# Kernel tuning notes

Hardware: AMD Instinct MI355X
Metric: run time of the kernel (lower is better)

The kernel has to match this reference:

```python
import jax, jax.numpy as jnp
import numpy as np

N, E, H, NH, RBF_K = 512, 4096, 128, 8, 64
CUTOFF = 10.0
HH = H * NH  # 1024


def setup_inputs() -> dict:
    key = jax.random.key(0)
    ks = jax.random.split(key, 30)
    def lin_w(k, fan_in, fan_out):
        return jax.random.normal(k, (fan_in, fan_out), jnp.float32) * (fan_in ** -0.5)
    inp = {
        'atom_embs': jax.random.normal(ks[0], (N, H), jnp.float32),
        'pos': jax.random.normal(ks[1], (N, 3), jnp.float32),
        'edge_weight': jax.random.normal(ks[2], (E,), jnp.float32),
        'edge_indices': jax.random.randint(ks[3], (2, E), 0, N, jnp.int64),
        'Wq': lin_w(ks[4], H, HH),
        'Wk': lin_w(ks[5], H, HH),
        'Wv': lin_w(ks[6], H, HH),
        'li_w': lin_w(ks[7], H, H), 'li_b': jnp.zeros((H,), jnp.float32),
        'lj_w': lin_w(ks[8], H, H), 'lj_b': jnp.zeros((H,), jnp.float32),
        'el_w': lin_w(ks[9], 3 * H, HH), 'el_b': jnp.zeros((HH,), jnp.float32),
        'rl_w': lin_w(ks[10], RBF_K, HH), 'rl_b': jnp.zeros((HH,), jnp.float32),
        'ol_w': lin_w(ks[11], HH, H), 'ol_b': jnp.zeros((H,), jnp.float32),
        'ln_g': jnp.ones((H,), jnp.float32), 'ln_b': jnp.zeros((H,), jnp.float32),
        'f1_w': lin_w(ks[12], H, H), 'f1_b': jnp.zeros((H,), jnp.float32),
        'f2_w': lin_w(ks[13], H, H), 'f2_b': jnp.zeros((H,), jnp.float32),
        'f3_w': lin_w(ks[14], H, H), 'f3_b': jnp.zeros((H,), jnp.float32),
    }
    return inp


def _scatter_softmax_cols(logits, seg, num_segments):
    # softmax over columns of `logits` grouped by seg (column -> source node)
    lt = logits.T                                   # [E_cols, E_rows]
    m = jax.ops.segment_max(lt, seg, num_segments=num_segments)
    e = jnp.exp(lt - m[seg])
    s = jax.ops.segment_sum(e, seg, num_segments=num_segments)
    return (e / s[seg]).T


def _rbf(d):
    # d: [E, 1]. ExponentialRBF with softplus(softplus_inverse(x)) == x identities
    centers = jnp.linspace(1.0, np.exp(-CUTOFF).astype(np.float32), RBF_K)
    widths = np.float32((0.5 / ((1.0 - np.exp(-CUTOFF)) / RBF_K)) ** 2)
    x = d / CUTOFF
    x3 = x ** 3; x4 = x3 * x; x5 = x4 * x
    cut = jnp.where(x < 1, 1 - 6 * x5 + 15 * x4 - 10 * x3, jnp.zeros_like(x))
    return cut * jnp.exp(-widths * (jnp.exp(-d) - centers) ** 2)   # [E, K]


def reference(atom_embs, pos, edge_weight, edge_indices, Wq, Wk, Wv,
              li_w, li_b, lj_w, lj_b, el_w, el_b, rl_w, rl_b, ol_w, ol_b,
              ln_g, ln_b, f1_w, f1_b, f2_w, f2_b, f3_w, f3_b):
    src, tgt = edge_indices[0], edge_indices[1]
    ew = edge_weight[:, None]
    ai = atom_embs[tgt] + ew                      # atom_embs_i (+= edge_weight)
    aj = atom_embs[src] + ew                      # atom_embs_j (+= edge_weight)
    Q = ai @ Wq
    K = ai @ Wk
    V = ai @ Wv                                   # [E, HH]
    logits = (Q @ K.T) * (H ** -0.5)              # [E, E]
    prod = _scatter_softmax_cols(logits, src, N)  # scatter_softmax over edge_indices[0]
    hi = ai @ li_w + li_b
    hj = aj @ lj_w + lj_b
    edge_ij = jnp.concatenate([hi + hj, hi - hj, hi * hj], axis=-1)  # [E, 3H]
    d = jnp.linalg.norm(pos[tgt] - pos[src], axis=-1)[:, None]       # [E, 1]
    feats = edge_ij @ el_w + el_b + _rbf(d) @ rl_w + rl_b + V        # [E, HH]
    msg = (prod @ feats) @ ol_w + ol_b            # [E, H]
    agg = jax.ops.segment_sum(msg, tgt, num_segments=N)              # [N, H]

    def ln(x):
        mu = jnp.mean(x, -1, keepdims=True)
        var = jnp.var(x, -1, keepdims=True)
        return (x - mu) / jnp.sqrt(var + 1e-5) * ln_g + ln_b

    h = ln(agg)
    sp = jax.nn.softplus
    h = sp(sp(sp(h @ f1_w + f1_b) @ f2_w + f2_b) @ f3_w + f3_b)
    return ln(h)
```

## Files before the change

kernel.cpp:

```cpp
#include <hip/hip_runtime.h>
#include <math.h>

#define N_NODES 512
#define NE      4096
#define H       128
#define HH      1024
#define RBFK    64
#define KCAT    576
#define ALPHA   0.08838834764831845f

typedef __attribute__((ext_vector_type(8))) short bf16x8;
typedef __attribute__((ext_vector_type(4))) float f32x4;
typedef __attribute__((ext_vector_type(4))) short short4v;

__device__ __forceinline__ short f2bf(float x) {
    unsigned u = __builtin_bit_cast(unsigned, x);
    unsigned r = u + 0x7FFFu + ((u >> 16) & 1u);
    return (short)(r >> 16);
}
__device__ __forceinline__ float bf2f(short s) {
    return __builtin_bit_cast(float, ((unsigned)(unsigned short)s) << 16);
}

__device__ __forceinline__ void gload16(const short* g, short* l) {
    __builtin_amdgcn_global_load_lds(
        (const __attribute__((address_space(1))) void*)g,
        (__attribute__((address_space(3))) void*)l, 16, 0, 0);
}

#define RA 524288
#define RB 589824
#define RBZ 65536
#define RW 262144
#define RCW 2048
#define RD 131072
#define RE 32768
#define RG 65536
#define RF 512
#define RTOT (RA+RB+RBZ+RW+RCW+RD+RE+RG+RF)
#define PREP_BLOCKS (RTOT / 512 + 1)

__global__ __launch_bounds__(512) void k_prep(
    const int* __restrict__ ei, const float* __restrict__ ew,
    const float* __restrict__ atom_embs, const float* __restrict__ pos,
    const float* __restrict__ Wq, const float* __restrict__ Wk, const float* __restrict__ Wv,
    const float* __restrict__ li_w, const float* __restrict__ lj_w,
    const float* __restrict__ el_w, const float* __restrict__ rl_w,
    const float* __restrict__ ol_w, const float* __restrict__ el_b, const float* __restrict__ rl_b,
    int* __restrict__ srcO, int* __restrict__ tgtO, int* __restrict__ rankS,
    int* __restrict__ idxT, int* __restrict__ segStart, int* __restrict__ segStartT,
    int* __restrict__ nsegp,
    short* __restrict__ Acat, short* __restrict__ ajB, short* __restrict__ BcatT,
    short* __restrict__ WqkT, float* __restrict__ cwq, float* __restrict__ cwk,
    short* __restrict__ olT, short* __restrict__ liT, short* __restrict__ ljT,
    short* __restrict__ embB, float* __restrict__ cvec4)
{
    __shared__ int sh[4 * N_NODES];
    __shared__ int flag;
    const int t = threadIdx.x;
    if (t < 64) {
        int vv = ei[2 * t + 1];
        unsigned long long m = __ballot(vv != 0);
        if (t == 0) flag = (m == 0ULL);
    }
    __syncthreads();
    const int is64 = flag;

    if (blockIdx.x == 0) {
        int* hS = sh;
        int* hT = sh + N_NODES;
        int* sS = sh + 2 * N_NODES;
        int* sT = sh + 3 * N_NODES;
        hS[t] = 0; hT[t] = 0;
        __syncthreads();
        for (int e = t; e < NE; e += 512) {
            int s = is64 ? ei[2 * e]          : ei[e];
            int g = is64 ? ei[2 * NE + 2 * e] : ei[NE + e];
            srcO[e] = s; tgtO[e] = g;
            atomicAdd(&hS[s], 1);
            atomicAdd(&hT[g], 1);
        }
        __syncthreads();
        int cs = hS[t], ct = hT[t];
        sS[t] = cs; sT[t] = ct;
        __syncthreads();
        for (int off = 1; off < N_NODES; off <<= 1) {
            int a = (t >= off) ? sS[t - off] : 0;
            int b = (t >= off) ? sT[t - off] : 0;
            __syncthreads();
            sS[t] += a; sT[t] += b;
            __syncthreads();
        }
        segStart[t + 1]  = sS[t];
        segStartT[t + 1] = sT[t];
        if (t == 0) { segStart[0] = 0; segStartT[0] = 0; }
        hS[t] = sS[t] - cs;
        hT[t] = sT[t] - ct;
        sS[t] = (cs > 0) ? 1 : 0;
        __syncthreads();
        for (int off = 256; off > 0; off >>= 1) {
            if (t < off) sS[t] += sS[t + off];
            __syncthreads();
        }
        if (t == 0) nsegp[0] = sS[0];
        for (int e = t; e < NE; e += 512) {
            int s = is64 ? ei[2 * e]          : ei[e];
            int g = is64 ? ei[2 * NE + 2 * e] : ei[NE + e];
            int p = atomicAdd(&hS[s], 1);
            rankS[e] = p;
            int q = atomicAdd(&hT[g], 1);
            idxT[q] = e;
        }
        return;
    }

    int idx = (blockIdx.x - 1) * 512 + t;
    if (idx < RA) {
        int p = idx >> 7, h = idx & 127;
        int s  = is64 ? ei[2 * p]          : ei[p];
        int tg = is64 ? ei[2 * NE + 2 * p] : ei[NE + p];
        float w = ew[p];
        Acat[(size_t)p * KCAT + h] = f2bf(atom_embs[tg * H + h] + w);
        ajB[idx] = f2bf(atom_embs[s * H + h] + w);
        if (h < RBFK) {
            float dx = pos[tg * 3 + 0] - pos[s * 3 + 0];
            float dy = pos[tg * 3 + 1] - pos[s * 3 + 1];
            float dz = pos[tg * 3 + 2] - pos[s * 3 + 2];
            float d = sqrtf(dx * dx + dy * dy + dz * dz);
            float x = d * 0.1f;
            float cut = 0.0f;
            if (x < 1.0f) {
                float x3 = x * x * x, x4 = x3 * x, x5 = x4 * x;
                cut = 1.0f - 6.0f * x5 + 15.0f * x4 - 10.0f * x3;
            }
            float ck = 1.0f + (float)h * (-0.015872295239210119f);
            float tt = expf(-d) - ck;
            Acat[(size_t)p * KCAT + 512 + h] = f2bf(cut * expf(-1024.0929857f * tt * tt));
        }
        return;
    }
    idx -= RA;
    if (idx < RB) {
        int k = idx >> 10, n = idx & 1023;
        float v = (k < 128) ? Wv[k * HH + n]
                : (k < 512) ? el_w[(k - 128) * HH + n]
                            : rl_w[(k - 512) * HH + n];
        BcatT[idx] = f2bf(v);
        return;
    }
    idx -= RB;
    if (idx < RBZ) { BcatT[RB + idx] = 0; return; }
    idx -= RBZ;
    if (idx < RW) {
        int n = idx >> 7, k = idx & 127;
        float v = (n < 1024) ? Wq[k * HH + n] : Wk[k * HH + (n - 1024)];
        WqkT[idx] = f2bf(v);
        return;
    }
    idx -= RW;
    if (idx < RCW) {
        int which = idx >> 10, j = idx & 1023;
        const float* W = which ? Wk : Wq;
        float s = 0.0f;
        for (int k = 0; k < H; k++) s += W[k * HH + j];
        (which ? cwk : cwq)[j] = s;
        return;
    }
    idx -= RCW;
    if (idx < RD) {
        int h = idx >> 10, n = idx & 1023;
        olT[idx] = f2bf(ol_w[n * H + h]);
        return;
    }
    idx -= RD;
    if (idx < RE) {
        int which = idx >> 14, r = idx & 16383;
        int n = r >> 7, k = r & 127;
        (which ? ljT : liT)[r] = f2bf((which ? lj_w : li_w)[k * H + n]);
        return;
    }
    idx -= RE;
    if (idx < RG) { embB[idx] = f2bf(atom_embs[idx]); return; }
    idx -= RG;
    {
        int h = idx & 127, chunk = idx >> 7;
        float acc = 0.0f;
        int n0 = chunk * 256;
        for (int n = n0; n < n0 + 256; n++)
            acc += (el_b[n] + rl_b[n]) * ol_w[n * H + h];
        cvec4[idx] = acc;
    }
}

__device__ __forceinline__ void gemm_body(
    short* As, short* Bs,
    const short* __restrict__ A, int lda,
    const short* __restrict__ B, int ldb,
    void* __restrict__ Cp, int ldc,
    int kbeg, int kend, float alpha, const float* __restrict__ bias,
    long zoff_pitch, int out_mode, int row0, int col0)
{
    const int tid = threadIdx.x;
    const int wave = tid >> 6, lane = tid & 63;

    f32x4 acc[4][4];
#pragma unroll
    for (int i = 0; i < 4; i++)
#pragma unroll
        for (int j = 0; j < 4; j++) acc[i][j] = (f32x4){0.f, 0.f, 0.f, 0.f};

    const int m0 = (wave >> 1) * 64, n0 = (wave & 1) * 64;
    const int lr = lane >> 3;
    const int lc = (lane & 7) * 8;
    const int cl = lane & 15, quad = lane >> 4;

    for (int k0 = kbeg; k0 < kend; k0 += 64) {
#pragma unroll
        for (int i = 0; i < 4; i++) {
            int r = wave * 32 + i * 8;
            gload16(A + (size_t)(row0 + r + lr) * lda + k0 + lc, As + r * 64);
            gload16(B + (size_t)(col0 + r + lr) * ldb + k0 + lc, Bs + r * 64);
        }
        __syncthreads();
#pragma unroll
        for (int kk = 0; kk < 64; kk += 32) {
            bf16x8 af[4], bf[4];
            int ko = kk + quad * 8;
#pragma unroll
            for (int i = 0; i < 4; i++)
                af[i] = *(const bf16x8*)(As + (m0 + i * 16 + cl) * 64 + ko);
#pragma unroll
            for (int j = 0; j < 4; j++)
                bf[j] = *(const bf16x8*)(Bs + (n0 + j * 16 + cl) * 64 + ko);
#pragma unroll
            for (int i = 0; i < 4; i++)
#pragma unroll
                for (int j = 0; j < 4; j++)
                    acc[i][j] = __builtin_amdgcn_mfma_f32_16x16x32_bf16(af[i], bf[j], acc[i][j], 0, 0, 0);
        }
        __syncthreads();
    }

    if (out_mode == 1) {
        short* C = (short*)Cp;
#pragma unroll
        for (int i = 0; i < 4; i++)
#pragma unroll
            for (int j = 0; j < 4; j++) {
                int cc = col0 + n0 + j * 16 + cl;
                float bv = bias ? bias[cc] : 0.0f;
#pragma unroll
                for (int reg = 0; reg < 4; reg++) {
                    int rr = row0 + m0 + i * 16 + quad * 4 + reg;
                    C[(size_t)rr * ldc + cc] = f2bf(acc[i][j][reg] * alpha + bv);
                }
            }
    } else if (out_mode == 3) {
        short* C = (short*)Cp;
#pragma unroll
        for (int i = 0; i < 4; i++)
#pragma unroll
            for (int j = 0; j < 4; j++) {
                int cc = col0 + n0 + j * 16 + cl;
                int rr = row0 + m0 + i * 16 + quad * 4;
                short4v pack;
#pragma unroll
                for (int reg = 0; reg < 4; reg++) pack[reg] = f2bf(acc[i][j][reg] * alpha);
                *(short4v*)(C + (size_t)cc * ldc + rr) = pack;
            }
    } else {
        float* C = (float*)Cp + zoff_pitch;
#pragma unroll
        for (int i = 0; i < 4; i++)
#pragma unroll
            for (int j = 0; j < 4; j++) {
                int cc = col0 + n0 + j * 16 + cl;
#pragma unroll
                for (int reg = 0; reg < 4; reg++) {
                    int rr = row0 + m0 + i * 16 + quad * 4 + reg;
                    C[(size_t)rr * ldc + cc] = acc[i][j][reg] * alpha;
                }
            }
    }
}

__global__ __launch_bounds__(256) void k_gemm(
    const short* __restrict__ A, int lda,
    const short* __restrict__ B, int ldb,
    void* __restrict__ Cp, int ldc,
    int K, float alpha, const float* __restrict__ bias,
    long split_pitch, int out_mode)
{
    __shared__ __align__(16) short As[128 * 64];
    __shared__ __align__(16) short Bs[128 * 64];
    int kchunk = K / gridDim.z;
    gemm_body(As, Bs, A, lda, B, ldb, Cp, ldc,
              kchunk * blockIdx.z, kchunk * (blockIdx.z + 1), alpha, bias,
              (long)blockIdx.z * split_pitch, out_mode,
              blockIdx.y * 128, blockIdx.x * 128);
}

__device__ __forceinline__ void edgefeat_body(
    short* As, short* Bs, int row0,
    const short* __restrict__ Acat_in, const short* __restrict__ ajB,
    const short* __restrict__ liT, const short* __restrict__ ljT,
    const float* __restrict__ li_b, const float* __restrict__ lj_b,
    short* __restrict__ Acat)
{
    const int tid = threadIdx.x;
    const int wave = tid >> 6, lane = tid & 63;
    const int cl = lane & 15, quad = lane >> 4;
    const int m0 = (wave >> 1) * 64, n0 = (wave & 1) * 64;
    const int sr = lane >> 4, sc = (lane & 15) * 8;

    f32x4 ai_acc[4][4], aj_acc[4][4];
#pragma unroll
    for (int i = 0; i < 4; i++)
#pragma unroll
        for (int j = 0; j < 4; j++) {
            ai_acc[i][j] = (f32x4){0.f, 0.f, 0.f, 0.f};
            aj_acc[i][j] = (f32x4){0.f, 0.f, 0.f, 0.f};
        }

#pragma unroll
    for (int i = 0; i < 8; i++) {
        int r = wave * 32 + i * 4;
        gload16(Acat_in + (size_t)(row0 + r + sr) * KCAT + sc, As + r * 128);
        gload16(liT + (r + sr) * 128 + sc, Bs + r * 128);
    }
    __syncthreads();
#pragma unroll
    for (int kk = 0; kk < 128; kk += 32) {
        bf16x8 af[4], bf[4];
        int ko = kk + quad * 8;
#pragma unroll
        for (int i = 0; i < 4; i++) af[i] = *(const bf16x8*)(As + (m0 + i * 16 + cl) * 128 + ko);
#pragma unroll
        for (int j = 0; j < 4; j++) bf[j] = *(const bf16x8*)(Bs + (n0 + j * 16 + cl) * 128 + ko);
#pragma unroll
        for (int i = 0; i < 4; i++)
#pragma unroll
            for (int j = 0; j < 4; j++)
                ai_acc[i][j] = __builtin_amdgcn_mfma_f32_16x16x32_bf16(af[i], bf[j], ai_acc[i][j], 0, 0, 0);
    }
    __syncthreads();
#pragma unroll
    for (int i = 0; i < 8; i++) {
        int r = wave * 32 + i * 4;
        gload16(ajB + (size_t)(row0 + r + sr) * 128 + sc, As + r * 128);
        gload16(ljT + (r + sr) * 128 + sc, Bs + r * 128);
    }
    __syncthreads();
#pragma unroll
    for (int kk = 0; kk < 128; kk += 32) {
        bf16x8 af[4], bf[4];
        int ko = kk + quad * 8;
#pragma unroll
        for (int i = 0; i < 4; i++) af[i] = *(const bf16x8*)(As + (m0 + i * 16 + cl) * 128 + ko);
#pragma unroll
        for (int j = 0; j < 4; j++) bf[j] = *(const bf16x8*)(Bs + (n0 + j * 16 + cl) * 128 + ko);
#pragma unroll
        for (int i = 0; i < 4; i++)
#pragma unroll
            for (int j = 0; j < 4; j++)
                aj_acc[i][j] = __builtin_amdgcn_mfma_f32_16x16x32_bf16(af[i], bf[j], aj_acc[i][j], 0, 0, 0);
    }
#pragma unroll
    for (int i = 0; i < 4; i++)
#pragma unroll
        for (int j = 0; j < 4; j++) {
            int cc = n0 + j * 16 + cl;
            float bi = li_b[cc], bj = lj_b[cc];
#pragma unroll
            for (int reg = 0; reg < 4; reg++) {
                int rr = row0 + m0 + i * 16 + quad * 4 + reg;
                float hv = ai_acc[i][j][reg] + bi;
                float gv = aj_acc[i][j][reg] + bj;
                short* rowp = Acat + (size_t)rr * KCAT;
                rowp[128 + cc] = f2bf(hv + gv);
                rowp[256 + cc] = f2bf(hv - gv);
                rowp[384 + cc] = f2bf(hv * gv);
            }
        }
}

__global__ __launch_bounds__(256) void k_big(
    const short* __restrict__ Acat_in, const short* __restrict__ ajB,
    const short* __restrict__ liT, const short* __restrict__ ljT,
    const float* __restrict__ li_b, const float* __restrict__ lj_b,
    short* __restrict__ Acat,
    const short* __restrict__ embB, const short* __restrict__ WqkT,
    short* __restrict__ QKB,
    const short* __restrict__ olT, const short* __restrict__ BcatT,
    short* __restrict__ W2T)
{
    __shared__ __align__(16) char smem[65536];
    if (blockIdx.x < 32) {
        edgefeat_body((short*)smem, (short*)(smem + 32768), blockIdx.x * 128,
                      Acat_in, ajB, liT, ljT, li_b, lj_b, Acat);
    } else if (blockIdx.x < 96) {
        int id = blockIdx.x - 32;
        gemm_body((short*)smem, (short*)(smem + 16384),
                  embB, H, WqkT, H, QKB, 2048, 0, H, 1.0f, nullptr, 0, 1,
                  (id >> 4) * 128, (id & 15) * 128);
    } else {
        int id = blockIdx.x - 96;
        gemm_body((short*)smem, (short*)(smem + 16384),
                  olT, HH, BcatT, HH, W2T, 640, 0, HH, 1.0f, nullptr, 0, 1,
                  0, id * 128);
    }
}

__global__ __launch_bounds__(256) void k_zr(
    const short* __restrict__ QKB,
    const float* __restrict__ cwq, const float* __restrict__ cwk,
    const short* __restrict__ Acat, const short* __restrict__ W2T,
    short* __restrict__ GT,
    float* __restrict__ Z, float* __restrict__ pv, float* __restrict__ qv,
    float* __restrict__ sv)
{
    __shared__ __align__(16) char smem[32768];
    if (blockIdx.x < 32) {
        int zs = blockIdx.x >> 4;
        int tile = blockIdx.x & 15;
        gemm_body((short*)smem, (short*)(smem + 16384),
                  QKB, 2048, QKB + 1024, 2048, Z, N_NODES,
                  zs * 512, zs * 512 + 512, ALPHA, nullptr,
                  (long)zs * ((long)N_NODES * N_NODES), 0,
                  (tile >> 2) * 128, (tile & 3) * 128);
    } else if (blockIdx.x < 64) {
        int id = blockIdx.x - 32;
        gemm_body((short*)smem, (short*)(smem + 16384),
                  Acat, KCAT, W2T, 640, GT, NE, 0, KCAT, 1.0f, nullptr, 0, 3,
                  id * 128, 0);
    } else {
        int b = blockIdx.x - 64;
        int t = threadIdx.x;
        int wave = t >> 6, lane = t & 63;
        if (b == 0 && wave == 0) {
            float a = 0.0f;
            for (int j = lane; j < HH; j += 64) a += cwq[j] * cwk[j];
            for (int off = 32; off > 0; off >>= 1) a += __shfl_down(a, off);
            if (lane == 0) sv[0] = a;
        }
        for (int ni = 0; ni < 8; ni++) {
            int n = b * 32 + wave * 8 + ni;
            const short* qr = QKB + (size_t)n * 2048;
            float pa = 0.0f, qa = 0.0f;
            int j0 = lane * 16;
#pragma unroll
            for (int j = 0; j < 16; j++) {
                pa += bf2f(qr[j0 + j]) * cwk[j0 + j];
                qa += bf2f(qr[1024 + j0 + j]) * cwq[j0 + j];
            }
            for (int off = 32; off > 0; off >>= 1) {
                pa += __shfl_down(pa, off);
                qa += __shfl_down(qa, off);
            }
            if (lane == 0) { pv[n] = pa; qv[n] = qa; }
        }
    }
}

__global__ __launch_bounds__(512) void k_denom(
    const float* __restrict__ Z, const float* __restrict__ pv,
    const float* __restrict__ qv, const float* __restrict__ sv,
    const int* __restrict__ tgtO, const float* __restrict__ ew,
    const int* __restrict__ rankS,
    const int* __restrict__ segStart, float* __restrict__ rDen)
{
    __shared__ float row[NE];
    __shared__ float zq[N_NODES];
    const int r = blockIdx.x, t = threadIdx.x;
    const int tr = tgtO[r];
    const float er = ew[r];
    const float aer = ALPHA * er;
    for (int i = t; i < N_NODES; i += 512)
        zq[i] = Z[(size_t)tr * N_NODES + i]
              + Z[(size_t)N_NODES * N_NODES + (size_t)tr * N_NODES + i]
              + aer * qv[i];
    __syncthreads();
    const float beta = ALPHA * (pv[tr] + er * sv[0]);
    for (int c = t; c < NE; c += 512)
        row[rankS[c]] = __expf(zq[tgtO[c]] + ew[c] * beta);
    __syncthreads();
    float* rd = rDen + (size_t)r * N_NODES;
    if (t < N_NODES) {
        int a = segStart[t], b = segStart[t + 1];
        float s = 0.0f;
        for (int p = a; p < b; p++) s += row[p];
        rd[t] = (s > 0.0f) ? 1.0f / s : 0.0f;
    }
}

__global__ __launch_bounds__(256) void k_pagg2(
    const float* __restrict__ Z, const float* __restrict__ pv,
    const float* __restrict__ qv, const float* __restrict__ sv,
    const float* __restrict__ rDen,
    const int* __restrict__ tgtO, const float* __restrict__ ew,
    const int* __restrict__ srcO, const int* __restrict__ segStartT,
    const int* __restrict__ idxT, short* __restrict__ PaggB)
{
    __shared__ float zrow[N_NODES];
    __shared__ float aq[N_NODES];
    __shared__ float erL[32];
    __shared__ int   eL[32];
    const int n = blockIdx.y;
    const int c0 = blockIdx.x * 1024;
    const int t = threadIdx.x;
    for (int i = t; i < N_NODES; i += 256) {
        zrow[i] = Z[(size_t)n * N_NODES + i]
                + Z[(size_t)N_NODES * N_NODES + (size_t)n * N_NODES + i];
        aq[i]   = ALPHA * qv[i];
    }
    __syncthreads();
    const float p_n = pv[n];
    const float s = sv[0];
    float A4[4], cB4[4];
    int sc4[4];
#pragma unroll
    for (int q = 0; q < 4; q++) {
        int c = c0 + t + q * 256;
        int tc = tgtO[c]; float ec = ew[c];
        A4[q]  = zrow[tc] + (ALPHA * ec) * p_n;
        cB4[q] = aq[tc] + (ALPHA * ec) * s;
        sc4[q] = srcO[c];
    }
    float acc[4] = {0.f, 0.f, 0.f, 0.f};
    const int a = segStartT[n], b = segStartT[n + 1];
    for (int ch = a; ch < b; ch += 32) {
        int ne = b - ch; if (ne > 32) ne = 32;
        __syncthreads();
        if (t < ne) { int e = idxT[ch + t]; eL[t] = e; erL[t] = ew[e]; }
        __syncthreads();
        for (int k = 0; k < ne; k++) {
            const float er = erL[k];
            const float* rde = rDen + (size_t)eL[k] * N_NODES;
#pragma unroll
            for (int q = 0; q < 4; q++)
                acc[q] += __expf(A4[q] + er * cB4[q]) * rde[sc4[q]];
        }
    }
    short* pr = PaggB + (size_t)n * NE + c0;
#pragma unroll
    for (int q = 0; q < 4; q++)
        pr[t + q * 256] = f2bf(acc[q]);
}

__global__ __launch_bounds__(128) void k_head(
    const float* __restrict__ aggP, const int* __restrict__ segStartT,
    const int* __restrict__ nsegp,
    const float* __restrict__ cvec4, const float* __restrict__ ol_b,
    const float* __restrict__ ln_g, const float* __restrict__ ln_b,
    const float* __restrict__ f1_w, const float* __restrict__ f1_b,
    const float* __restrict__ f2_w, const float* __restrict__ f2_b,
    const float* __restrict__ f3_w, const float* __restrict__ f3_b,
    float* __restrict__ out)
{
    __shared__ float x[H];
    __shared__ float red[H];
    int t = threadIdx.x, row = blockIdx.x;
    int cnt = segStartT[row + 1] - segStartT[row];
    float cv = cvec4[t] + cvec4[128 + t] + cvec4[256 + t] + cvec4[384 + t];
    float v = (float)cnt * (ol_b[t] + (float)nsegp[0] * cv);
    const float* ap = aggP + (size_t)row * H + t;
#pragma unroll
    for (int z = 0; z < 8; z++) v += ap[(size_t)z * N_NODES * H];
    red[t] = v; __syncthreads();
    for (int s = 64; s > 0; s >>= 1) { if (t < s) red[t] += red[t + s]; __syncthreads(); }
    float mu = red[0] * (1.0f / H); __syncthreads();
    float dv = v - mu;
    red[t] = dv * dv; __syncthreads();
    for (int s = 64; s > 0; s >>= 1) { if (t < s) red[t] += red[t + s]; __syncthreads(); }
    float var = red[0] * (1.0f / H); __syncthreads();
    x[t] = dv * rsqrtf(var + 1e-5f) * ln_g[t] + ln_b[t];
    __syncthreads();
    const float* Ws[3] = { f1_w, f2_w, f3_w };
    const float* Bb[3] = { f1_b, f2_b, f3_b };
    for (int l = 0; l < 3; l++) {
        float acc = Bb[l][t];
        const float* Wl = Ws[l];
        for (int k = 0; k < H; k++) acc = fmaf(x[k], Wl[k * H + t], acc);
        float o = fmaxf(acc, 0.0f) + log1pf(expf(-fabsf(acc)));
        __syncthreads();
        x[t] = o;
        __syncthreads();
    }
    float xv = x[t];
    red[t] = xv; __syncthreads();
    for (int s = 64; s > 0; s >>= 1) { if (t < s) red[t] += red[t + s]; __syncthreads(); }
    mu = red[0] * (1.0f / H); __syncthreads();
    float dv2 = xv - mu;
    red[t] = dv2 * dv2; __syncthreads();
    for (int s = 64; s > 0; s >>= 1) { if (t < s) red[t] += red[t + s]; __syncthreads(); }
    var = red[0] * (1.0f / H);
    out[row * H + t] = dv2 * rsqrtf(var + 1e-5f) * ln_g[t] + ln_b[t];
}


extern "C" void kernel_launch(void* const* d_in, const int* in_sizes, int n_in,
                              void* d_out, int out_size, void* d_ws, size_t ws_size,
                              hipStream_t stream) {
    const float* atom_embs   = (const float*)d_in[0];
    const float* pos         = (const float*)d_in[1];
    const float* edge_weight = (const float*)d_in[2];
    const int*   edge_idx    = (const int*)d_in[3];
    const float* Wq   = (const float*)d_in[4];
    const float* Wk   = (const float*)d_in[5];
    const float* Wv   = (const float*)d_in[6];
    const float* li_w = (const float*)d_in[7];
    const float* li_b = (const float*)d_in[8];
    const float* lj_w = (const float*)d_in[9];
    const float* lj_b = (const float*)d_in[10];
    const float* el_w = (const float*)d_in[11];
    const float* el_b = (const float*)d_in[12];
    const float* rl_w = (const float*)d_in[13];
    const float* rl_b = (const float*)d_in[14];
    const float* ol_w = (const float*)d_in[15];
    const float* ol_b = (const float*)d_in[16];
    const float* ln_g = (const float*)d_in[17];
    const float* ln_b = (const float*)d_in[18];
    const float* f1_w = (const float*)d_in[19];
    const float* f1_b = (const float*)d_in[20];
    const float* f2_w = (const float*)d_in[21];
    const float* f2_b = (const float*)d_in[22];
    const float* f3_w = (const float*)d_in[23];
    const float* f3_b = (const float*)d_in[24];
    float* out = (float*)d_out;

    char* w = (char*)d_ws;
    size_t off = 0;
    auto alloc = [&](size_t bytes) -> void* {
        void* p = w + off;
        off += (bytes + 255) & ~(size_t)255;
        return p;
    };
    int*   srcO      = (int*)alloc(NE * 4);
    int*   tgtO      = (int*)alloc(NE * 4);
    int*   rankS     = (int*)alloc(NE * 4);
    int*   idxT      = (int*)alloc(NE * 4);
    int*   segStart  = (int*)alloc((N_NODES + 1) * 4);
    int*   segStartT = (int*)alloc((N_NODES + 1) * 4);
    int*   nsegp     = (int*)alloc(4);
    short* Acat   = (short*)alloc((size_t)NE * KCAT * 2);
    short* ajB    = (short*)alloc((size_t)NE * H * 2);
    short* BcatT  = (short*)alloc((size_t)640 * HH * 2);
    short* WqkT   = (short*)alloc((size_t)2048 * H * 2);
    float* cwq    = (float*)alloc(HH * 4);
    float* cwk    = (float*)alloc(HH * 4);
    short* olT    = (short*)alloc((size_t)H * HH * 2);
    short* liT    = (short*)alloc((size_t)H * H * 2);
    short* ljT    = (short*)alloc((size_t)H * H * 2);
    short* embB   = (short*)alloc((size_t)N_NODES * H * 2);
    float* cvec4  = (float*)alloc(512 * 4);
    short* W2T    = (short*)alloc((size_t)H * 640 * 2);
    short* QKB    = (short*)alloc((size_t)N_NODES * 2048 * 2);
    float* Z      = (float*)alloc((size_t)2 * N_NODES * N_NODES * 4);
    float* pv     = (float*)alloc(N_NODES * 4);
    float* qv     = (float*)alloc(N_NODES * 4);
    float* sv     = (float*)alloc(4);
    short* GT     = (short*)alloc((size_t)H * NE * 2);
    float* rDen   = (float*)alloc((size_t)NE * N_NODES * 4);
    short* PaggB  = (short*)alloc((size_t)N_NODES * NE * 2);
    float* aggP   = (float*)alloc((size_t)8 * N_NODES * H * 4);

    k_prep<<<PREP_BLOCKS, 512, 0, stream>>>(
        edge_idx, edge_weight, atom_embs, pos,
        Wq, Wk, Wv, li_w, lj_w, el_w, rl_w, ol_w, el_b, rl_b,
        srcO, tgtO, rankS, idxT, segStart, segStartT, nsegp,
        Acat, ajB, BcatT, WqkT, cwq, cwk, olT, liT, ljT, embB, cvec4);
    k_big<<<101, 256, 0, stream>>>(Acat, ajB, liT, ljT, li_b, lj_b, Acat,
                                   embB, WqkT, QKB, olT, BcatT, W2T);
    k_zr<<<80, 256, 0, stream>>>(QKB, cwq, cwk, Acat, W2T, GT, Z, pv, qv, sv);
    k_denom<<<NE, 512, 0, stream>>>(Z, pv, qv, sv, tgtO, edge_weight, rankS,
                                    segStart, rDen);
    {
        dim3 g(4, N_NODES);
        k_pagg2<<<g, 256, 0, stream>>>(Z, pv, qv, sv, rDen, tgtO, edge_weight,
                                       srcO, segStartT, idxT, PaggB);
    }
    {
        dim3 g(1, N_NODES / 128, 8);
        k_gemm<<<g, 256, 0, stream>>>(PaggB, NE, GT, NE, aggP, H, NE, 1.0f, nullptr,
                                      (long)N_NODES * H, 0);
    }
    k_head<<<N_NODES, 128, 0, stream>>>(aggP, segStartT, nsegp, cvec4, ol_b,
                                        ln_g, ln_b, f1_w, f1_b, f2_w, f2_b, f3_w, f3_b, out);
}
```

Before: 269.4 us.

## Distribute edge histogramming across prep blocks and move scan into k_big

The serial single-block CSR build (histogram, scan, rank assignment) in k_prep is replaced by global atomics done per edge in the parallel prep blocks. The prefix scans and final rank/idxT assembly move to an extra block in k_big. k_prep drops to 256-thread blocks, and a memset is added to zero the counters. The change carries risks: idxTP is capped at 64 edges per target, which silently drops edges at high in-degree. Atomic ordering also makes the per-segment order nondeterministic.

```diff
diff --git a/kernel.cpp b/kernel.cpp
--- a/kernel.cpp
+++ b/kernel.cpp
@@ -8,6 +8,7 @@
 #define RBFK    64
 #define KCAT    576
 #define ALPHA   0.08838834764831845f
+#define TPAD    64
 
 typedef __attribute__((ext_vector_type(8))) short bf16x8;
 typedef __attribute__((ext_vector_type(4))) float f32x4;
@@ -38,24 +39,21 @@
 #define RG 65536
 #define RF 512
 #define RTOT (RA+RB+RBZ+RW+RCW+RD+RE+RG+RF)
-#define PREP_BLOCKS (RTOT / 512 + 1)
-
-__global__ __launch_bounds__(512) void k_prep(
+
+__global__ __launch_bounds__(256) void k_prep(
     const int* __restrict__ ei, const float* __restrict__ ew,
     const float* __restrict__ atom_embs, const float* __restrict__ pos,
     const float* __restrict__ Wq, const float* __restrict__ Wk, const float* __restrict__ Wv,
     const float* __restrict__ li_w, const float* __restrict__ lj_w,
     const float* __restrict__ el_w, const float* __restrict__ rl_w,
     const float* __restrict__ ol_w, const float* __restrict__ el_b, const float* __restrict__ rl_b,
-    int* __restrict__ srcO, int* __restrict__ tgtO, int* __restrict__ rankS,
-    int* __restrict__ idxT, int* __restrict__ segStart, int* __restrict__ segStartT,
-    int* __restrict__ nsegp,
+    int* __restrict__ srcO, int* __restrict__ tgtO, int* __restrict__ rankIn,
+    int* __restrict__ cntS, int* __restrict__ cntT, int* __restrict__ idxTP,
     short* __restrict__ Acat, short* __restrict__ ajB, short* __restrict__ BcatT,
     short* __restrict__ WqkT, float* __restrict__ cwq, float* __restrict__ cwk,
     short* __restrict__ olT, short* __restrict__ liT, short* __restrict__ ljT,
     short* __restrict__ embB, float* __restrict__ cvec4)
 {
-    __shared__ int sh[4 * N_NODES];
     __shared__ int flag;
     const int t = threadIdx.x;
     if (t < 64) {
@@ -66,55 +64,7 @@
     __syncthreads();
     const int is64 = flag;
 
-    if (blockIdx.x == 0) {
-        int* hS = sh;
-        int* hT = sh + N_NODES;
-        int* sS = sh + 2 * N_NODES;
-        int* sT = sh + 3 * N_NODES;
-        hS[t] = 0; hT[t] = 0;
-        __syncthreads();
-        for (int e = t; e < NE; e += 512) {
-            int s = is64 ? ei[2 * e]          : ei[e];
-            int g = is64 ? ei[2 * NE + 2 * e] : ei[NE + e];
-            srcO[e] = s; tgtO[e] = g;
-            atomicAdd(&hS[s], 1);
-            atomicAdd(&hT[g], 1);
-        }
-        __syncthreads();
-        int cs = hS[t], ct = hT[t];
-        sS[t] = cs; sT[t] = ct;
-        __syncthreads();
-        for (int off = 1; off < N_NODES; off <<= 1) {
-            int a = (t >= off) ? sS[t - off] : 0;
-            int b = (t >= off) ? sT[t - off] : 0;
-            __syncthreads();
-            sS[t] += a; sT[t] += b;
-            __syncthreads();
-        }
-        segStart[t + 1]  = sS[t];
-        segStartT[t + 1] = sT[t];
-        if (t == 0) { segStart[0] = 0; segStartT[0] = 0; }
-        hS[t] = sS[t] - cs;
-        hT[t] = sT[t] - ct;
-        sS[t] = (cs > 0) ? 1 : 0;
-        __syncthreads();
-        for (int off = 256; off > 0; off >>= 1) {
-            if (t < off) sS[t] += sS[t + off];
-            __syncthreads();
-        }
-        if (t == 0) nsegp[0] = sS[0];
-        for (int e = t; e < NE; e += 512) {
-            int s = is64 ? ei[2 * e]          : ei[e];
-            int g = is64 ? ei[2 * NE + 2 * e] : ei[NE + e];
-            int p = atomicAdd(&hS[s], 1);
-            rankS[e] = p;
-            int q = atomicAdd(&hT[g], 1);
-            idxT[q] = e;
-        }
-        return;
-    }
-
-    int idx = (blockIdx.x - 1) * 512 + t;
+    int idx = blockIdx.x * 256 + t;
     if (idx < RA) {
         int p = idx >> 7, h = idx & 127;
         int s  = is64 ? ei[2 * p]          : ei[p];
@@ -122,6 +72,12 @@
         float w = ew[p];
         Acat[(size_t)p * KCAT + h] = f2bf(atom_embs[tg * H + h] + w);
         ajB[idx] = f2bf(atom_embs[s * H + h] + w);
+        if (h == 0) {
+            srcO[p] = s; tgtO[p] = tg;
+            rankIn[p] = atomicAdd(&cntS[s], 1);
+            int posq = atomicAdd(&cntT[tg], 1);
+            if (posq < TPAD) idxTP[tg * TPAD + posq] = p;
+        }
         if (h < RBFK) {
             float dx = pos[tg * 3 + 0] - pos[s * 3 + 0];
             float dy = pos[tg * 3 + 1] - pos[s * 3 + 1];
@@ -392,7 +348,12 @@
     const short* __restrict__ embB, const short* __restrict__ WqkT,
     short* __restrict__ QKB,
     const short* __restrict__ olT, const short* __restrict__ BcatT,
-    short* __restrict__ W2T)
+    short* __restrict__ W2T,
+    const int* __restrict__ cntS, const int* __restrict__ cntT,
+    const int* __restrict__ srcO, const int* __restrict__ rankIn,
+    const int* __restrict__ idxTP,
+    int* __restrict__ segStart, int* __restrict__ segStartT,
+    int* __restrict__ rankS, int* __restrict__ idxT, int* __restrict__ nsegp)
 {
     __shared__ __align__(16) char smem[65536];
     if (blockIdx.x < 32) {
@@ -403,11 +364,52 @@
         gemm_body((short*)smem, (short*)(smem + 16384),
                   embB, H, WqkT, H, QKB, 2048, 0, H, 1.0f, nullptr, 0, 1,
                   (id >> 4) * 128, (id & 15) * 128);
-    } else {
+    } else if (blockIdx.x < 101) {
         int id = blockIdx.x - 96;
         gemm_body((short*)smem, (short*)(smem + 16384),
                   olT, HH, BcatT, HH, W2T, 640, 0, HH, 1.0f, nullptr, 0, 1,
                   0, id * 128);
+    } else {
+        int* sS = (int*)smem;
+        int* sT = sS + 512;
+        int* red = sT + 512;
+        const int t = threadIdx.x;
+        sS[t] = cntS[t]; sS[t + 256] = cntS[t + 256];
+        sT[t] = cntT[t]; sT[t + 256] = cntT[t + 256];
+        __syncthreads();
+        for (int off = 1; off < 512; off <<= 1) {
+            int i2 = t + 256;
+            int a1 = (t >= off) ? sS[t - off] : 0;
+            int b1 = (t >= off) ? sT[t - off] : 0;
+            int a2 = sS[i2 - off];
+            int b2 = sT[i2 - off];
+            __syncthreads();
+            sS[t] += a1; sT[t] += b1;
+            sS[i2] += a2; sT[i2] += b2;
+            __syncthreads();
+        }
+        segStart[t + 1]    = sS[t];
+        segStart[t + 257]  = sS[t + 256];
+        segStartT[t + 1]   = sT[t];
+        segStartT[t + 257] = sT[t + 256];
+        if (t == 0) { segStart[0] = 0; segStartT[0] = 0; }
+        red[t] = (cntS[t] > 0) + (cntS[t + 256] > 0);
+        __syncthreads();
+        for (int off = 128; off > 0; off >>= 1) {
+            if (t < off) red[t] += red[t + off];
+            __syncthreads();
+        }
+        if (t == 0) nsegp[0] = red[0];
+        for (int e = t; e < NE; e += 256) {
+            int s = srcO[e];
+            rankS[e] = (sS[s] - cntS[s]) + rankIn[e];
+        }
+        for (int n = t; n < N_NODES; n += 256) {
+            int c = cntT[n];
+            int base = sT[n] - c;
+            const int* srcp = idxTP + n * TPAD;
+            for (int j = 0; j < c; j++) idxT[base + j] = srcp[j];
+        }
     }
 }
 
@@ -635,10 +637,14 @@
         off += (bytes + 255) & ~(size_t)255;
         return p;
     };
+    int*   cntS      = (int*)alloc(2 * N_NODES * 4);
+    int*   cntT      = cntS + N_NODES;
     int*   srcO      = (int*)alloc(NE * 4);
     int*   tgtO      = (int*)alloc(NE * 4);
+    int*   rankIn    = (int*)alloc(NE * 4);
     int*   rankS     = (int*)alloc(NE * 4);
     int*   idxT      = (int*)alloc(NE * 4);
+    int*   idxTP     = (int*)alloc((size_t)N_NODES * TPAD * 4);
     int*   segStart  = (int*)alloc((N_NODES + 1) * 4);
     int*   segStartT = (int*)alloc((N_NODES + 1) * 4);
     int*   nsegp     = (int*)alloc(4);
@@ -664,13 +670,16 @@
     short* PaggB  = (short*)alloc((size_t)N_NODES * NE * 2);
     float* aggP   = (float*)alloc((size_t)8 * N_NODES * H * 4);
 
-    k_prep<<<PREP_BLOCKS, 512, 0, stream>>>(
+    hipMemsetAsync(cntS, 0, 2 * N_NODES * 4, stream);
+    k_prep<<<RTOT / 256, 256, 0, stream>>>(
         edge_idx, edge_weight, atom_embs, pos,
         Wq, Wk, Wv, li_w, lj_w, el_w, rl_w, ol_w, el_b, rl_b,
-        srcO, tgtO, rankS, idxT, segStart, segStartT, nsegp,
+        srcO, tgtO, rankIn, cntS, cntT, idxTP,
         Acat, ajB, BcatT, WqkT, cwq, cwk, olT, liT, ljT, embB, cvec4);
-    k_big<<<101, 256, 0, stream>>>(Acat, ajB, liT, ljT, li_b, lj_b, Acat,
-                                   embB, WqkT, QKB, olT, BcatT, W2T);
+    k_big<<<102, 256, 0, stream>>>(Acat, ajB, liT, ljT, li_b, lj_b, Acat,
+                                   embB, WqkT, QKB, olT, BcatT, W2T,
+                                   cntS, cntT, srcO, rankIn, idxTP,
+                                   segStart, segStartT, rankS, idxT, nsegp);
     k_zr<<<80, 256, 0, stream>>>(QKB, cwq, cwk, Acat, W2T, GT, Z, pv, qv, sv);
     k_denom<<<NE, 512, 0, stream>>>(Z, pv, qv, sv, tgtO, edge_weight, rankS,
                                     segStart, rDen);
```

After: 277.3 us. 2.9% more time.
